# Optimization experiments

Measured on AMD Instinct MI355X. Metric: run time of the kernel, lower is better.

Reference implementation:

```python
import jax, jax.numpy as jnp
import numpy as np

H = 1152  # hidden_size
NH = 16   # num_attention_heads
HD = H // NH  # head_dim = 72
FF = 4304  # intermediate_size
EPS = 1e-6
S = 4096
B = 1
NDOCS = 32


def _linear_params(key, d_in, d_out):
    kw, kb = jax.random.split(key)
    lim = 1.0 / np.sqrt(d_in)
    w = jax.random.uniform(kw, (d_out, d_in), jnp.float32, -lim, lim)
    b = jax.random.uniform(kb, (d_out,), jnp.float32, -lim, lim)
    return w, b


def setup_inputs() -> dict:
    key = jax.random.key(0)
    ks = jax.random.split(key, 8)
    hidden_states = jax.random.normal(ks[0], (B, S, H), jnp.float32)
    document_ids = jnp.sort(jax.random.randint(ks[1], (S,), 0, NDOCS))
    q_w, q_b = _linear_params(ks[2], H, H)
    k_w, k_b = _linear_params(ks[3], H, H)
    v_w, v_b = _linear_params(ks[4], H, H)
    o_w, o_b = _linear_params(ks[5], H, H)
    fc1_w, fc1_b = _linear_params(ks[6], H, FF)
    fc2_w, fc2_b = _linear_params(ks[7], FF, H)
    return {
        'hidden_states': hidden_states,
        'document_ids': document_ids,
        'q_w': q_w, 'q_b': q_b, 'k_w': k_w, 'k_b': k_b,
        'v_w': v_w, 'v_b': v_b, 'o_w': o_w, 'o_b': o_b,
        'ln1_g': jnp.ones((H,), jnp.float32), 'ln1_b': jnp.zeros((H,), jnp.float32),
        'ln2_g': jnp.ones((H,), jnp.float32), 'ln2_b': jnp.zeros((H,), jnp.float32),
        'fc1_w': fc1_w, 'fc1_b': fc1_b, 'fc2_w': fc2_w, 'fc2_b': fc2_b,
    }


def _layer_norm(x, g, b):
    mu = jnp.mean(x, axis=-1, keepdims=True)
    var = jnp.mean(jnp.square(x - mu), axis=-1, keepdims=True)
    return (x - mu) * jax.lax.rsqrt(var + EPS) * g + b


def _forward(hidden_states, q_w, q_b, k_w, k_b, v_w, v_b, o_w, o_b,
             ln1_g, ln1_b, ln2_g, ln2_b, fc1_w, fc1_b, fc2_w, fc2_b,
             document_ids):
    b, s, _ = hidden_states.shape
    scale = HD ** -0.5

    residual = hidden_states
    x = _layer_norm(hidden_states, ln1_g, ln1_b)

    # projections (torch Linear: y = x @ W.T + b)
    q = (x @ q_w.T + q_b).reshape(b, s, NH, HD).transpose(0, 2, 1, 3)
    k = (x @ k_w.T + k_b).reshape(b, s, NH, HD).transpose(0, 2, 1, 3)
    v = (x @ v_w.T + v_b).reshape(b, s, NH, HD).transpose(0, 2, 1, 3)

    # document-masked attention: attend only within same document id
    scores = jnp.einsum('bhqd,bhkd->bhqk', q, k) * scale
    mask = document_ids[:, None] == document_ids[None, :]  # [s, s]
    scores = jnp.where(mask[None, None], scores, -jnp.inf)
    attn = jax.nn.softmax(scores, axis=-1)
    out = jnp.einsum('bhqk,bhkd->bhqd', attn, v)  # [b,h,s,d]
    out = out.transpose(0, 2, 1, 3).reshape(b, s, H)
    out = out @ o_w.T + o_b

    hidden = residual + out
    residual = hidden
    x = _layer_norm(hidden, ln2_g, ln2_b)
    x = jax.nn.gelu(x @ fc1_w.T + fc1_b, approximate=True)
    x = x @ fc2_w.T + fc2_b
    return residual + x


def reference(hidden_states, document_ids, q_w, q_b, k_w, k_b, v_w, v_b,
              o_w, o_b, ln1_g, ln1_b, ln2_g, ln2_b, fc1_w, fc1_b, fc2_w, fc2_b):
    return _forward(hidden_states, q_w, q_b, k_w, k_b, v_w, v_b, o_w, o_b,
                    ln1_g, ln1_b, ln2_g, ln2_b, fc1_w, fc1_b, fc2_w, fc2_b,
                    document_ids)
```

## Files before the change

### kernel.cpp

```cpp
#include <hip/hip_runtime.h>

typedef unsigned short u16;
typedef unsigned int u32;
typedef __attribute__((ext_vector_type(8))) __bf16 bf16x8;
typedef __attribute__((ext_vector_type(8))) u16 u16x8;
typedef __attribute__((ext_vector_type(4))) float f32x4;
typedef __attribute__((ext_vector_type(2))) u32 u32x2;

#define SEQ 4096
#define HID 1152
#define NHEAD 16
#define HDIM 72
#define FF 4304
#define FFP 4352
#define H3 3456

__device__ __forceinline__ u16 f2bf(float f) {
  u32 u = __builtin_bit_cast(u32, f);
  u32 r = u + 0x7fffu + ((u >> 16) & 1u);
  return (u16)(r >> 16);
}
__device__ __forceinline__ float bf2f(u16 h) {
  return __builtin_bit_cast(float, (u32)h << 16);
}
__device__ __forceinline__ float bflo(u32 u) { return __builtin_bit_cast(float, u << 16); }
__device__ __forceinline__ float bfhi(u32 u) { return __builtin_bit_cast(float, u & 0xffff0000u); }

typedef const __attribute__((address_space(1))) void* gas_t;
typedef __attribute__((address_space(3))) void* las_t;
__device__ __forceinline__ void load_lds16(const void* g, void* l) {
  __builtin_amdgcn_global_load_lds((gas_t)(unsigned long long)g,
                                   (las_t)(u32)(unsigned long long)l, 16, 0, 0);
}

__device__ __forceinline__ float gelu_fast(float x) {
  float z = 0.7978845608f * (x + 0.044715f * x * x * x);
  return x / (1.f + __expf(-2.f * z));
}

__global__ __launch_bounds__(256) void cvt4x4_k(const float* __restrict__ a,
                                                const float* __restrict__ b,
                                                const float* __restrict__ c,
                                                const float* __restrict__ d,
                                                u16* __restrict__ out, int n4) {
  int i = blockIdx.x * 256 + threadIdx.x;
  if (i >= n4) return;
  const float* in = (blockIdx.y == 0) ? a : (blockIdx.y == 1) ? b : (blockIdx.y == 2) ? c : d;
  f32x4 f = ((const f32x4*)in)[i];
  u32x2 o;
  o[0] = (u32)f2bf(f[0]) | ((u32)f2bf(f[1]) << 16);
  o[1] = (u32)f2bf(f[2]) | ((u32)f2bf(f[3]) << 16);
  ((u32x2*)(out + (size_t)blockIdx.y * n4 * 4))[i] = o;
}

__global__ __launch_bounds__(256) void cvt4_pad_k(const float* __restrict__ in,
                                                  u16* __restrict__ out,
                                                  int rows, int sc, int dc) {
  int i = blockIdx.x * 256 + threadIdx.x;
  long long n4 = (long long)rows * dc / 4;
  if (i >= n4) return;
  long long idx = (long long)i * 4;
  int r = (int)(idx / dc);
  int c = (int)(idx % dc);
  u32x2 o;
  if (c < sc) {
    f32x4 f = *(const f32x4*)(in + (size_t)r * sc + c);
    o[0] = (u32)f2bf(f[0]) | ((u32)f2bf(f[1]) << 16);
    o[1] = (u32)f2bf(f[2]) | ((u32)f2bf(f[3]) << 16);
  } else {
    o[0] = 0; o[1] = 0;
  }
  ((u32x2*)out)[i] = o;
}

__global__ __launch_bounds__(256) void prep_k(const int* __restrict__ ids,
                                              const float* __restrict__ qb,
                                              const float* __restrict__ kb,
                                              const float* __restrict__ vb,
                                              const float* __restrict__ f1b,
                                              int* __restrict__ se,
                                              float* __restrict__ bqkv,
                                              float* __restrict__ bf1,
                                              float* __restrict__ zbuf) {
  int i = blockIdx.x * 256 + threadIdx.x;
  if (i < H3) bqkv[i] = (i < HID) ? qb[i] : (i < 2 * HID ? kb[i - HID] : vb[i - 2 * HID]);
  if (i < FFP) bf1[i] = (i < FF) ? f1b[i] : 0.f;
  if (i < 16) zbuf[i] = 0.f;
  if (i < SEQ) {
    int id = ids[i];
    int lo = 0, hi = SEQ;
    while (lo < hi) { int mid = (lo + hi) >> 1; if (ids[mid] < id) lo = mid + 1; else hi = mid; }
    int s = lo;
    lo = 0; hi = SEQ;
    while (lo < hi) { int mid = (lo + hi) >> 1; if (ids[mid] <= id) lo = mid + 1; else hi = mid; }
    se[2 * i] = s;
    se[2 * i + 1] = lo;
  }
}

__global__ __launch_bounds__(256) void ln_k(const float* __restrict__ x,
                                            const float* __restrict__ g,
                                            const float* __restrict__ b,
                                            u16* __restrict__ y) {
  __shared__ float sred[8];
  int row = blockIdx.x, tid = threadIdx.x;
  const f32x4* xr = (const f32x4*)(x + (size_t)row * HID);
  f32x4 v0 = {}, v1 = {};
  float s = 0.f, s2 = 0.f;
  int c0 = tid, c1 = tid + 256;
  v0 = xr[c0];
  if (c1 < 288) v1 = xr[c1];
#pragma unroll
  for (int j = 0; j < 4; ++j) { s += v0[j] + v1[j]; s2 += v0[j] * v0[j] + v1[j] * v1[j]; }
#pragma unroll
  for (int sh = 32; sh; sh >>= 1) { s += __shfl_xor(s, sh); s2 += __shfl_xor(s2, sh); }
  if ((tid & 63) == 0) { sred[tid >> 6] = s; sred[4 + (tid >> 6)] = s2; }
  __syncthreads();
  s = sred[0] + sred[1] + sred[2] + sred[3];
  s2 = sred[4] + sred[5] + sred[6] + sred[7];
  float mu = s * (1.f / HID);
  float rs = rsqrtf(s2 * (1.f / HID) - mu * mu + 1e-6f);
  u16* yr = y + (size_t)row * HID;
  const f32x4* g4 = (const f32x4*)g;
  const f32x4* b4 = (const f32x4*)b;
  {
    f32x4 gv = g4[c0], bv = b4[c0];
    u32x2 o;
    o[0] = (u32)f2bf((v0[0] - mu) * rs * gv[0] + bv[0]) |
           ((u32)f2bf((v0[1] - mu) * rs * gv[1] + bv[1]) << 16);
    o[1] = (u32)f2bf((v0[2] - mu) * rs * gv[2] + bv[2]) |
           ((u32)f2bf((v0[3] - mu) * rs * gv[3] + bv[3]) << 16);
    *(u32x2*)(yr + c0 * 4) = o;
  }
  if (c1 < 288) {
    f32x4 gv = g4[c1], bv = b4[c1];
    u32x2 o;
    o[0] = (u32)f2bf((v1[0] - mu) * rs * gv[0] + bv[0]) |
           ((u32)f2bf((v1[1] - mu) * rs * gv[1] + bv[1]) << 16);
    o[1] = (u32)f2bf((v1[2] - mu) * rs * gv[2] + bv[2]) |
           ((u32)f2bf((v1[3] - mu) * rs * gv[3] + bv[3]) << 16);
    *(u32x2*)(yr + c1 * 4) = o;
  }
}

template <int EP>
__global__ __launch_bounds__(256, 3) void gemm_bt(const u16* __restrict__ A,
                                                  const u16* __restrict__ B,
                                                  void* __restrict__ outp,
                                                  const float* __restrict__ bias,
                                                  const float* __restrict__ resid,
                                                  int M, int N, int K) {
  __shared__ u16 As[3 * 128 * 32];
  __shared__ u16 Bs[3 * 128 * 32];
  int tid = threadIdx.x;
  int l = tid & 63, w = tid >> 6;
  int nxy = gridDim.x * gridDim.y;
  int bidf = blockIdx.y * gridDim.x + blockIdx.x;
  int cpx = nxy >> 3;
  bidf = (bidf & 7) * cpx + (bidf >> 3);
  int m0 = (bidf / gridDim.x) * 128;
  int n0 = (bidf % gridDim.x) * 128;
  int wr = w >> 1, wc = w & 1;
  f32x4 acc[4][4] = {};
  int sr = tid >> 2, sc = tid & 3;
  int row0 = sr, row1 = 64 + sr;
  int x0 = ((row0 >> 1) & 3) ^ (((row0 >> 3) & 1) << 1);
  int x1 = ((row1 >> 1) & 3) ^ (((row1 >> 3) & 1) << 1);
  const char* Ag0 = (const char*)A + ((size_t)(m0 + row0) * K + (size_t)((sc ^ x0) * 8)) * 2;
  const char* Ag1 = (const char*)A + ((size_t)(m0 + row1) * K + (size_t)((sc ^ x1) * 8)) * 2;
  const char* Bg0 = (const char*)B + ((size_t)(n0 + row0) * K + (size_t)((sc ^ x0) * 8)) * 2;
  const char* Bg1 = (const char*)B + ((size_t)(n0 + row1) * K + (size_t)((sc ^ x1) * 8)) * 2;
  char* AsB = (char*)As;
  char* BsB = (char*)Bs;
  int xl = (((l & 15) >> 1) & 3) ^ ((((l & 15) >> 3) & 1) << 1);
  int cfr = ((l >> 4) ^ xl) * 16;
  const char* ArB = (const char*)As + (wr * 64 + (l & 15)) * 64 + cfr;
  const char* BrB = (const char*)Bs + (wc * 64 + (l & 15)) * 64 + cfr;
  int k0 = 0, kend = K;
  if (EP == 5) {
    int nz = gridDim.z;
    int ksp = ((K / 32 + nz - 1) / nz) * 32;
    k0 = blockIdx.z * ksp;
    kend = min(K, k0 + ksp);
  }
  int nsteps = (kend - k0) / 32;
  {
    size_t kb0 = (size_t)k0 * 2;
    load_lds16(Ag0 + kb0, AsB + tid * 16);
    load_lds16(Ag1 + kb0, AsB + 4096 + tid * 16);
    load_lds16(Bg0 + kb0, BsB + tid * 16);
    load_lds16(Bg1 + kb0, BsB + 4096 + tid * 16);
    size_t kb1 = (size_t)(k0 + 32) * 2;
    load_lds16(Ag0 + kb1, AsB + 8192 + tid * 16);
    load_lds16(Ag1 + kb1, AsB + 8192 + 4096 + tid * 16);
    load_lds16(Bg0 + kb1, BsB + 8192 + tid * 16);
    load_lds16(Bg1 + kb1, BsB + 8192 + 4096 + tid * 16);
  }
  int buf = 0;
  for (int t = 0; t < nsteps; ++t) {
    if (t + 2 < nsteps) {
      int nb = buf >= 1 ? buf - 1 : 2;
      size_t kb = (size_t)(k0 + (t + 2) * 32) * 2;
      load_lds16(Ag0 + kb, AsB + nb * 8192 + tid * 16);
      load_lds16(Ag1 + kb, AsB + nb * 8192 + 4096 + tid * 16);
      load_lds16(Bg0 + kb, BsB + nb * 8192 + tid * 16);
      load_lds16(Bg1 + kb, BsB + nb * 8192 + 4096 + tid * 16);
      asm volatile("s_waitcnt vmcnt(4)" ::: "memory");
    } else {
      asm volatile("s_waitcnt vmcnt(0)" ::: "memory");
    }
    __builtin_amdgcn_sched_barrier(0);
    __builtin_amdgcn_s_barrier();
    __builtin_amdgcn_sched_barrier(0);
    {
      const char* Ar = ArB + buf * 8192;
      const char* Br = BrB + buf * 8192;
      bf16x8 af[4], bfr[4];
#pragma unroll
      for (int m = 0; m < 4; ++m) af[m] = *(const bf16x8*)(Ar + m * 1024);
#pragma unroll
      for (int n = 0; n < 4; ++n) bfr[n] = *(const bf16x8*)(Br + n * 1024);
#pragma unroll
      for (int m = 0; m < 4; ++m)
#pragma unroll
        for (int n = 0; n < 4; ++n)
          acc[m][n] = __builtin_amdgcn_mfma_f32_16x16x32_bf16(af[m], bfr[n], acc[m][n], 0, 0, 0);
    }
    __builtin_amdgcn_sched_barrier(0);
    __builtin_amdgcn_s_barrier();
    __builtin_amdgcn_sched_barrier(0);
    buf = buf == 2 ? 0 : buf + 1;
  }
#pragma unroll
  for (int m = 0; m < 4; ++m) {
    int row = m0 + wr * 64 + m * 16 + (l >> 4) * 4;
#pragma unroll
    for (int n = 0; n < 4; ++n) {
      int col = n0 + wc * 64 + n * 16 + (l & 15);
      float bv = (EP == 5) ? 0.f : bias[col];
      if (EP == 4) {
        int region = (col >= 2304) ? 2 : (col >= 1152 ? 1 : 0);
        int cw = col - region * 1152;
        int hh = cw / 72;
        int dd = cw - hh * 72;
        u16* dst = (u16*)outp + (((size_t)region * NHEAD + hh) * SEQ) * HDIM + dd;
#pragma unroll
        for (int j = 0; j < 4; ++j)
          dst[(size_t)(row + j) * HDIM] = f2bf(acc[m][n][j] + bv);
      } else if (EP == 5) {
        u16* P = (u16*)outp + (size_t)blockIdx.z * M * N;
#pragma unroll
        for (int j = 0; j < 4; ++j)
          P[(size_t)(row + j) * N + col] = f2bf(acc[m][n][j]);
      } else {
#pragma unroll
        for (int j = 0; j < 4; ++j) {
          size_t idx = (size_t)(row + j) * N + col;
          float v = acc[m][n][j] + bv;
          if (EP == 1) ((u16*)outp)[idx] = f2bf(gelu_fast(v));
          else ((float*)outp)[idx] = v + resid[idx];
        }
      }
    }
  }
}

template <int NS>
__global__ __launch_bounds__(256) void splitk_reduce_k(const u16* __restrict__ P,
                                                       const float* __restrict__ bias,
                                                       const float* __restrict__ resid,
                                                       float* __restrict__ out, int n4) {
  int i = blockIdx.x * 256 + threadIdx.x;
  if (i >= n4) return;
  size_t base = (size_t)i * 4;
  int col = (int)(base % HID);
  f32x4 a = {};
#pragma unroll
  for (int s = 0; s < NS; ++s) {
    u32x2 pv = *(const u32x2*)(P + (size_t)s * SEQ * HID + base);
    a[0] += bflo(pv[0]);
    a[1] += bfhi(pv[0]);
    a[2] += bflo(pv[1]);
    a[3] += bfhi(pv[1]);
  }
  f32x4 bv = *(const f32x4*)(bias + col);
  f32x4 rv = ((const f32x4*)resid)[i];
  ((f32x4*)out)[i] = a + bv + rv;
}

__device__ __forceinline__ u32 swz(u32 a) { return a ^ (((a >> 8) & 7u) << 4); }

__global__ __launch_bounds__(256, 2) void attn_mfma_k(const u16* __restrict__ qkvh,
                                                      const int* __restrict__ se,
                                                      const float* __restrict__ zb,
                                                      u16* __restrict__ outb) {
  __shared__ u16 Ks[128 * 104];
  __shared__ u16 Vt[80 * 128];
  __shared__ u16 Ps[4][16 * 128];
  __shared__ int Sq[64], Eq[64];
  int tid = threadIdx.x, l = tid & 63, w = tid >> 6;
  int h = blockIdx.y, q0 = blockIdx.x * 64;
  const float scale = 0.1178511302f;
  const u16* Qh = qkvh + (size_t)h * SEQ * HDIM;
  const u16* Kh = qkvh + ((size_t)NHEAD + h) * SEQ * HDIM;
  const u16* Vh = qkvh + ((size_t)2 * NHEAD + h) * SEQ * HDIM;

  for (int i = tid; i < 512; i += 256) ((u32*)(Vt + 72 * 128))[i] = 0;

#pragma unroll
  for (int it = 0; it < 4; ++it) {
    int cw0 = it * 256 + w * 64;
    if (cw0 < 832) {
      int chunk = cw0 + l;
      int row = chunk / 13, c16 = chunk - row * 13;
      const void* src = (c16 < 9)
                            ? (const void*)(Qh + ((size_t)(q0 + row)) * HDIM + c16 * 8)
                            : (const void*)zb;
      load_lds16(src, (char*)Ks + (size_t)cw0 * 16);
    }
  }
  if (tid < 64) { Sq[tid] = se[2 * (q0 + tid)]; Eq[tid] = se[2 * (q0 + tid) + 1]; }
  __syncthreads();

  int sqj[4], eqj[4];
#pragma unroll
  for (int j = 0; j < 4; ++j) {
    int ql = w * 16 + (l >> 4) * 4 + j;
    sqj[j] = Sq[ql]; eqj[j] = Eq[ql];
  }
  const char* Aq = (const char*)Ks + (w * 16 + (l & 15)) * 208 + (l >> 4) * 16;
  bf16x8 aq[3];
#pragma unroll
  for (int dsl = 0; dsl < 3; ++dsl) aq[dsl] = *(const bf16x8*)(Aq + dsl * 64);
  __syncthreads();

  int kmin = se[2 * q0];
  int kmax = se[2 * (q0 + 63) + 1];
  f32x4 o[5] = {};
  float m_run[4], l_run[4];
#pragma unroll
  for (int j = 0; j < 4; ++j) { m_run[j] = -1e30f; l_run[j] = 0.f; }

  for (int kc = kmin; kc < kmax; kc += 128) {
#pragma unroll
    for (int it = 0; it < 7; ++it) {
      int cw0 = it * 256 + w * 64;
      if (cw0 < 1664) {
        int chunk = cw0 + l;
        int row = chunk / 13, c16 = chunk - row * 13;
        int krow = kc + row;
        const void* src = (c16 < 9 && krow < SEQ)
                              ? (const void*)(Kh + (size_t)krow * HDIM + c16 * 8)
                              : (const void*)zb;
        load_lds16(src, (char*)Ks + (size_t)cw0 * 16);
      }
    }
#pragma unroll
    for (int it = 0; it < 3; ++it) {
      int idx = it * 256 + tid;
      if (idx < 576) {
        int k2 = idx / 9, d8 = idx - k2 * 9;
        int kr0 = kc + 2 * k2, kr1 = kr0 + 1;
        kr0 = kr0 < SEQ ? kr0 : SEQ - 1;
        kr1 = kr1 < SEQ ? kr1 : SEQ - 1;
        u16x8 r0 = *(const u16x8*)(Vh + (size_t)kr0 * HDIM + d8 * 8);
        u16x8 r1 = *(const u16x8*)(Vh + (size_t)kr1 * HDIM + d8 * 8);
#pragma unroll
        for (int j = 0; j < 8; ++j) {
          u32 pr = (u32)r0[j] | ((u32)r1[j] << 16);
          *(u32*)((char*)Vt + swz((u32)(d8 * 8 + j) * 256 + (u32)k2 * 4)) = pr;
        }
      }
    }
    __syncthreads();

    f32x4 sf[8];
#pragma unroll
    for (int kt = 0; kt < 8; ++kt) {
      const char* Bk = (const char*)Ks + (kt * 16 + (l & 15)) * 208 + (l >> 4) * 16;
      f32x4 acc = {};
      acc = __builtin_amdgcn_mfma_f32_16x16x32_bf16(aq[0], *(const bf16x8*)Bk, acc, 0, 0, 0);
      acc = __builtin_amdgcn_mfma_f32_16x16x32_bf16(aq[1], *(const bf16x8*)(Bk + 64), acc, 0, 0, 0);
      acc = __builtin_amdgcn_mfma_f32_16x16x32_bf16(aq[2], *(const bf16x8*)(Bk + 128), acc, 0, 0, 0);
      sf[kt] = acc;
    }
    float mx[4] = {-1e30f, -1e30f, -1e30f, -1e30f};
#pragma unroll
    for (int kt = 0; kt < 8; ++kt) {
      int key = kc + kt * 16 + (l & 15);
#pragma unroll
      for (int j = 0; j < 4; ++j) {
        float s = sf[kt][j] * scale;
        bool valid = (key >= sqj[j]) && (key < eqj[j]);
        s = valid ? s : -1e30f;
        sf[kt][j] = s;
        mx[j] = fmaxf(mx[j], s);
      }
    }
#pragma unroll
    for (int j = 0; j < 4; ++j) {
      float m = mx[j];
      m = fmaxf(m, __shfl_xor(m, 1));
      m = fmaxf(m, __shfl_xor(m, 2));
      m = fmaxf(m, __shfl_xor(m, 4));
      m = fmaxf(m, __shfl_xor(m, 8));
      mx[j] = m;
    }
    float fz[4], ps[4];
#pragma unroll
    for (int j = 0; j < 4; ++j) {
      float mn = fmaxf(m_run[j], mx[j]);
      fz[j] = __expf(m_run[j] - mn);
      m_run[j] = mn;
      ps[j] = 0.f;
    }
#pragma unroll
    for (int kt = 0; kt < 8; ++kt)
#pragma unroll
      for (int j = 0; j < 4; ++j) {
        float s = sf[kt][j];
        float p = (s > -1e29f) ? __expf(s - m_run[j]) : 0.f;
        sf[kt][j] = p;
        ps[j] += p;
      }
#pragma unroll
    for (int j = 0; j < 4; ++j) {
      float p = ps[j];
      p += __shfl_xor(p, 1);
      p += __shfl_xor(p, 2);
      p += __shfl_xor(p, 4);
      p += __shfl_xor(p, 8);
      l_run[j] = l_run[j] * fz[j] + p;
#pragma unroll
      for (int dt = 0; dt < 5; ++dt) o[dt][j] *= fz[j];
    }
    char* PB = (char*)Ps[w];
#pragma unroll
    for (int kt = 0; kt < 8; ++kt)
#pragma unroll
      for (int j = 0; j < 4; ++j) {
        u32 a = (u32)((l >> 4) * 4 + j) * 256 + (u32)(kt * 16 + (l & 15)) * 2;
        *(u16*)(PB + swz(a)) = f2bf(sf[kt][j]);
      }
#pragma unroll
    for (int ks = 0; ks < 4; ++ks) {
      u32 aa = (u32)(l & 15) * 256 + (u32)((l >> 4) * 8 + ks * 32) * 2;
      bf16x8 ap = *(const bf16x8*)(PB + swz(aa));
#pragma unroll
      for (int dt = 0; dt < 5; ++dt) {
        u32 ba = (u32)(dt * 16 + (l & 15)) * 256 + (u32)((l >> 4) * 8 + ks * 32) * 2;
        bf16x8 bv = *(const bf16x8*)((const char*)Vt + swz(ba));
        o[dt] = __builtin_amdgcn_mfma_f32_16x16x32_bf16(ap, bv, o[dt], 0, 0, 0);
      }
    }
    __syncthreads();
  }

  float inv[4];
#pragma unroll
  for (int j = 0; j < 4; ++j) inv[j] = 1.f / l_run[j];
#pragma unroll
  for (int dt = 0; dt < 5; ++dt) {
    int d = dt * 16 + (l & 15);
    if (d < HDIM) {
#pragma unroll
      for (int j = 0; j < 4; ++j) {
        int q = q0 + w * 16 + (l >> 4) * 4 + j;
        outb[(size_t)q * HID + h * HDIM + d] = f2bf(o[dt][j] * inv[j]);
      }
    }
  }
}

constexpr size_t SZ_WQKV = (size_t)H3 * HID * 2;
constexpr size_t SZ_WO   = (size_t)HID * HID * 2;
constexpr size_t SZ_WF1  = (size_t)FFP * HID * 2;
constexpr size_t SZ_WF2  = (size_t)HID * FFP * 2;
constexpr size_t OFF_WQKV = 0;
constexpr size_t OFF_WO   = OFF_WQKV + SZ_WQKV;
constexpr size_t OFF_WF1  = OFF_WO + SZ_WO;
constexpr size_t OFF_BQKV = OFF_WF1 + SZ_WF1;
constexpr size_t OFF_BF1  = OFF_BQKV + (size_t)H3 * 4;
constexpr size_t OFF_SE   = OFF_BF1 + (size_t)FFP * 4;
constexpr size_t OFF_ZB   = OFF_SE + (size_t)SEQ * 2 * 4;
constexpr size_t OFF_XLN  = OFF_ZB + 64;
constexpr size_t OFF_QKV  = OFF_XLN + (size_t)SEQ * HID * 2;
constexpr size_t OFF_ACT  = OFF_QKV;
constexpr size_t OFF_AOUT = OFF_QKV + (size_t)SEQ * H3 * 2;
constexpr size_t OFF_HD   = OFF_AOUT + (size_t)SEQ * HID * 2;
constexpr size_t OFF_WF2  = OFF_HD + (size_t)SEQ * HID * 4;
constexpr size_t WS_NEED  = OFF_WF2 + SZ_WF2;
constexpr size_t OFF_P    = 0;
static_assert(OFF_ACT + (size_t)SEQ * FFP * 2 <= OFF_HD, "ACT must not clobber HD");
static_assert(3 * (size_t)SEQ * HID * 2 <= OFF_QKV, "P must stay in dead prefix");

extern "C" void kernel_launch(void* const* d_in, const int* in_sizes, int n_in,
                              void* d_out, int out_size, void* d_ws, size_t ws_size,
                              hipStream_t stream) {
  const float* hs   = (const float*)d_in[0];
  const int*   ids  = (const int*)d_in[1];
  const float* q_w  = (const float*)d_in[2];
  const float* q_b  = (const float*)d_in[3];
  const float* k_w  = (const float*)d_in[4];
  const float* k_b  = (const float*)d_in[5];
  const float* v_w  = (const float*)d_in[6];
  const float* v_b  = (const float*)d_in[7];
  const float* o_w  = (const float*)d_in[8];
  const float* o_b  = (const float*)d_in[9];
  const float* ln1g = (const float*)d_in[10];
  const float* ln1b = (const float*)d_in[11];
  const float* ln2g = (const float*)d_in[12];
  const float* ln2b = (const float*)d_in[13];
  const float* f1w  = (const float*)d_in[14];
  const float* f1b  = (const float*)d_in[15];
  const float* f2w  = (const float*)d_in[16];
  const float* f2b  = (const float*)d_in[17];

  if (ws_size < WS_NEED) return;

  char* ws = (char*)d_ws;
  u16*   Wqkv = (u16*)(ws + OFF_WQKV);
  u16*   Wf1  = (u16*)(ws + OFF_WF1);
  u16*   Wf2  = (u16*)(ws + OFF_WF2);
  float* Bqkv = (float*)(ws + OFF_BQKV);
  float* Bf1  = (float*)(ws + OFF_BF1);
  int*   SE   = (int*)(ws + OFF_SE);
  float* ZB   = (float*)(ws + OFF_ZB);
  u16*   XLN  = (u16*)(ws + OFF_XLN);
  u16*   QKVh = (u16*)(ws + OFF_QKV);
  u16*   ACT  = (u16*)(ws + OFF_ACT);
  u16*   AOUT = (u16*)(ws + OFF_AOUT);
  float* HD   = (float*)(ws + OFF_HD);
  u16*   Pp   = (u16*)(ws + OFF_P);
  u16*   Wo   = (u16*)(ws + OFF_WO);

  prep_k<<<dim3((FFP + 255) / 256), dim3(256), 0, stream>>>(ids, q_b, k_b, v_b, f1b, SE, Bqkv,
                                                            Bf1, ZB);
  int nW = HID * HID;
  cvt4x4_k<<<dim3(nW / 4 / 256, 4), dim3(256), 0, stream>>>(q_w, k_w, v_w, o_w, Wqkv, nW / 4);
  {
    int n4 = FFP * HID / 4;
    cvt4_pad_k<<<dim3((n4 + 255) / 256), dim3(256), 0, stream>>>(f1w, Wf1, 1, FF * HID, FFP * HID);
  }
  {
    int n4 = HID * FFP / 4;
    cvt4_pad_k<<<dim3((n4 + 255) / 256), dim3(256), 0, stream>>>(f2w, Wf2, HID, FF, FFP);
  }

  ln_k<<<dim3(SEQ), dim3(256), 0, stream>>>(hs, ln1g, ln1b, XLN);
  gemm_bt<4><<<dim3(H3 / 128, SEQ / 128), dim3(256), 0, stream>>>(XLN, Wqkv, QKVh, Bqkv, nullptr,
                                                                  SEQ, H3, HID);
  attn_mfma_k<<<dim3(SEQ / 64, NHEAD), dim3(256), 0, stream>>>(QKVh, SE, ZB, AOUT);
  gemm_bt<2><<<dim3(HID / 128, SEQ / 128), dim3(256), 0, stream>>>(AOUT, Wo, HD, o_b, hs,
                                                                   SEQ, HID, HID);
  ln_k<<<dim3(SEQ), dim3(256), 0, stream>>>(HD, ln2g, ln2b, XLN);
  gemm_bt<1><<<dim3(FFP / 128, SEQ / 128), dim3(256), 0, stream>>>(XLN, Wf1, ACT, Bf1, nullptr,
                                                                   SEQ, FFP, HID);
  gemm_bt<5><<<dim3(HID / 128, SEQ / 128, 3), dim3(256), 0, stream>>>(ACT, Wf2, Pp, nullptr,
                                                                      nullptr, SEQ, HID, FFP);
  splitk_reduce_k<3><<<dim3(SEQ * HID / 4 / 256), dim3(256), 0, stream>>>(Pp, f2b, HD,
                                                                          (float*)d_out,
                                                                          SEQ * HID / 4);
}
```

Baseline: 286.2 us.

## Deepen GEMM LDS pipeline to five buffers and drop trailing barrier

The GEMM now uses five LDS stages with a prefetch distance of three instead of three stages with distance two, so it can remove the second per-iteration barrier while keeping a spare buffer as a guard against write-after-read hazards. It also raises wave priority around the MFMA block and lowers the occupancy hint from three to two blocks per CU. The larger LDS footprint (80KB per block) and the lower occupancy hint trade latency hiding across blocks for deeper in-block prefetch and fewer synchronisations.

```diff
diff --git a/kernel.cpp b/kernel.cpp
--- a/kernel.cpp
+++ b/kernel.cpp
@@ -144,14 +144,14 @@
 }
 
 template <int EP>
-__global__ __launch_bounds__(256, 3) void gemm_bt(const u16* __restrict__ A,
+__global__ __launch_bounds__(256, 2) void gemm_bt(const u16* __restrict__ A,
                                                   const u16* __restrict__ B,
                                                   void* __restrict__ outp,
                                                   const float* __restrict__ bias,
                                                   const float* __restrict__ resid,
                                                   int M, int N, int K) {
-  __shared__ u16 As[3 * 128 * 32];
-  __shared__ u16 Bs[3 * 128 * 32];
+  __shared__ u16 As[5 * 128 * 32];
+  __shared__ u16 Bs[5 * 128 * 32];
   int tid = threadIdx.x;
   int l = tid & 63, w = tid >> 6;
   int nxy = gridDim.x * gridDim.y;
@@ -184,28 +184,29 @@
     kend = min(K, k0 + ksp);
   }
   int nsteps = (kend - k0) / 32;
-  {
-    size_t kb0 = (size_t)k0 * 2;
-    load_lds16(Ag0 + kb0, AsB + tid * 16);
-    load_lds16(Ag1 + kb0, AsB + 4096 + tid * 16);
-    load_lds16(Bg0 + kb0, BsB + tid * 16);
-    load_lds16(Bg1 + kb0, BsB + 4096 + tid * 16);
-    size_t kb1 = (size_t)(k0 + 32) * 2;
-    load_lds16(Ag0 + kb1, AsB + 8192 + tid * 16);
-    load_lds16(Ag1 + kb1, AsB + 8192 + 4096 + tid * 16);
-    load_lds16(Bg0 + kb1, BsB + 8192 + tid * 16);
-    load_lds16(Bg1 + kb1, BsB + 8192 + 4096 + tid * 16);
+#pragma unroll
+  for (int tt = 0; tt < 3; ++tt) {
+    size_t kb = (size_t)(k0 + tt * 32) * 2;
+    char* sa = AsB + tt * 8192;
+    char* sb = BsB + tt * 8192;
+    load_lds16(Ag0 + kb, sa + tid * 16);
+    load_lds16(Ag1 + kb, sa + 4096 + tid * 16);
+    load_lds16(Bg0 + kb, sb + tid * 16);
+    load_lds16(Bg1 + kb, sb + 4096 + tid * 16);
   }
   int buf = 0;
   for (int t = 0; t < nsteps; ++t) {
-    if (t + 2 < nsteps) {
-      int nb = buf >= 1 ? buf - 1 : 2;
-      size_t kb = (size_t)(k0 + (t + 2) * 32) * 2;
-      load_lds16(Ag0 + kb, AsB + nb * 8192 + tid * 16);
-      load_lds16(Ag1 + kb, AsB + nb * 8192 + 4096 + tid * 16);
-      load_lds16(Bg0 + kb, BsB + nb * 8192 + tid * 16);
-      load_lds16(Bg1 + kb, BsB + nb * 8192 + 4096 + tid * 16);
-      asm volatile("s_waitcnt vmcnt(4)" ::: "memory");
+    if (t + 3 < nsteps) {
+      int nb = buf + 3;
+      if (nb >= 5) nb -= 5;
+      size_t kb = (size_t)(k0 + (t + 3) * 32) * 2;
+      char* sa = AsB + nb * 8192;
+      char* sb = BsB + nb * 8192;
+      load_lds16(Ag0 + kb, sa + tid * 16);
+      load_lds16(Ag1 + kb, sa + 4096 + tid * 16);
+      load_lds16(Bg0 + kb, sb + tid * 16);
+      load_lds16(Bg1 + kb, sb + 4096 + tid * 16);
+      asm volatile("s_waitcnt vmcnt(8)" ::: "memory");
     } else {
       asm volatile("s_waitcnt vmcnt(0)" ::: "memory");
     }
@@ -220,16 +221,16 @@
       for (int m = 0; m < 4; ++m) af[m] = *(const bf16x8*)(Ar + m * 1024);
 #pragma unroll
       for (int n = 0; n < 4; ++n) bfr[n] = *(const bf16x8*)(Br + n * 1024);
+      __builtin_amdgcn_s_setprio(1);
 #pragma unroll
       for (int m = 0; m < 4; ++m)
 #pragma unroll
         for (int n = 0; n < 4; ++n)
           acc[m][n] = __builtin_amdgcn_mfma_f32_16x16x32_bf16(af[m], bfr[n], acc[m][n], 0, 0, 0);
+      __builtin_amdgcn_s_setprio(0);
     }
     __builtin_amdgcn_sched_barrier(0);
-    __builtin_amdgcn_s_barrier();
-    __builtin_amdgcn_sched_barrier(0);
-    buf = buf == 2 ? 0 : buf + 1;
+    buf = buf == 4 ? 0 : buf + 1;
   }
 #pragma unroll
   for (int m = 0; m < 4; ++m) {
```

Measured after the change: 286.7 us. No clear change (+0.2%).
